# Kernel tuning notes

Measured on AMD Instinct MI355X. Metric: run time of the kernel, lower is better.

## Reference

```python
import jax, jax.numpy as jnp
import numpy as np

N_ENT = 500000
N_REL = 64
E_DIM = 128
R_DIM = 128
REG_LAMBDA = 1e-5
M = 8192


def setup_inputs() -> dict:
    key = jax.random.key(0)
    k1, k2, k3, k4, k5, k6, k7 = jax.random.split(key, 7)
    # Xavier-uniform-ish init for relation_weight; normal for embeddings (nn.Embedding default)
    gain = float(np.sqrt(2.0))  # calculate_gain('relu')
    bound = gain * float(np.sqrt(6.0 / (E_DIM + R_DIM)))
    return {
        "h": jax.random.randint(k1, (M,), 0, N_ENT),
        "r": jax.random.randint(k2, (M,), 0, N_REL),
        "pos_t": jax.random.randint(k3, (M,), 0, N_ENT),
        "neg_t": jax.random.randint(k4, (M,), 0, N_ENT),
        "entity_embed": jax.random.normal(k5, (N_ENT, E_DIM), dtype=jnp.float32),
        "relation_embed": jax.random.normal(k6, (N_REL, R_DIM), dtype=jnp.float32),
        "relation_weight": jax.random.uniform(k7, (N_REL, E_DIM, R_DIM), dtype=jnp.float32, minval=-bound, maxval=bound),
    }


def _l2_norm(x):
    # sum over feature dim, halved -> shape (M,)
    return jnp.sum(x * x, axis=1) / 2.0


def reference(h, r, pos_t, neg_t, entity_embed, relation_embed, relation_weight):
    h_embed = entity_embed[h]            # (M, E)
    r_embed = relation_embed[r]          # (M, R)
    pos_t_embed = entity_embed[pos_t]    # (M, E)
    neg_t_embed = entity_embed[neg_t]    # (M, E)

    W = relation_weight[r]               # (M, E, R) relation-indexed gather
    h_vec = jnp.einsum('me,mer->mr', h_embed, W)
    pos_t_vec = jnp.einsum('me,mer->mr', pos_t_embed, W)
    neg_t_vec = jnp.einsum('me,mer->mr', neg_t_embed, W)

    pos_score = _l2_norm(h_vec + r_embed - pos_t_vec)
    neg_score = _l2_norm(h_vec + r_embed - neg_t_vec)
    kg_loss = jnp.mean(-jax.nn.log_sigmoid(pos_score - neg_score))

    kg_reg_loss = (jnp.mean(_l2_norm(h_embed)) + jnp.mean(_l2_norm(r_embed))
                   + jnp.mean(_l2_norm(pos_t_embed)) + jnp.mean(_l2_norm(neg_t_embed)))
    return kg_loss + REG_LAMBDA * kg_reg_loss
```

## Files before the change

### kernel.cpp

```cpp
#include <hip/hip_runtime.h>
#include <math.h>

#define E_DIM 128
#define R_DIM 128
#define N_REL 64
#define REG_LAMBDA 1e-5f

#define NSEG 32
#define GMAX 8
#define LISTMAX 512

__global__ void __launch_bounds__(128)
kge_grouped_kernel(const int* __restrict__ h_idx, const int* __restrict__ r_idx,
                   const int* __restrict__ pt_idx, const int* __restrict__ nt_idx,
                   const float* __restrict__ ent,
                   const float* __restrict__ rel,
                   const float* __restrict__ W,
                   float* __restrict__ per_sample,
                   int M)
{
    const int t      = threadIdx.x;
    const int rel_id = blockIdx.x >> 5;
    const int seg    = blockIdx.x & (NSEG - 1);

    __shared__ int s_cnt;
    __shared__ int s_list[LISTMAX];
    __shared__ __align__(16) float sh[GMAX][E_DIM];
    __shared__ __align__(16) float sp[GMAX][E_DIM];
    __shared__ __align__(16) float sn[GMAX][E_DIM];
    __shared__ float wpart[3][GMAX][2];

    const int range = (M + NSEG - 1) / NSEG;
    const int m0 = seg * range;
    const int m1 = min(m0 + range, M);

    if (t == 0) s_cnt = 0;
    __syncthreads();
    for (int m = m0 + t; m < m1; m += 128) {
        if (r_idx[m] == rel_id) {
            int p = atomicAdd(&s_cnt, 1);
            s_list[p] = m;
        }
    }
    __syncthreads();
    const int cnt = s_cnt;
    if (cnt == 0) return;

    const float* __restrict__ Wr = W + (size_t)rel_id * (E_DIM * R_DIM);
    const float re = rel[(size_t)rel_id * R_DIM + t];

    for (int c0 = 0; c0 < cnt; c0 += GMAX) {
#pragma unroll
        for (int g = 0; g < GMAX; ++g) {
            int sl = c0 + g; if (sl > cnt - 1) sl = cnt - 1;
            int m = s_list[sl];
            sh[g][t] = ent[(size_t)h_idx[m]  * E_DIM + t];
            sp[g][t] = ent[(size_t)pt_idx[m] * E_DIM + t];
            sn[g][t] = ent[(size_t)nt_idx[m] * E_DIM + t];
        }
        __syncthreads();

        float ah[GMAX], ap[GMAX], an[GMAX];
#pragma unroll
        for (int g = 0; g < GMAX; ++g) { ah[g] = 0.f; ap[g] = 0.f; an[g] = 0.f; }

#pragma unroll 2
        for (int e0 = 0; e0 < E_DIM; e0 += 4) {
            float w0 = Wr[(size_t)(e0 + 0) * R_DIM + t];
            float w1 = Wr[(size_t)(e0 + 1) * R_DIM + t];
            float w2 = Wr[(size_t)(e0 + 2) * R_DIM + t];
            float w3 = Wr[(size_t)(e0 + 3) * R_DIM + t];
#pragma unroll
            for (int g = 0; g < GMAX; ++g) {
                float4 h4 = *(const float4*)&sh[g][e0];
                float4 p4 = *(const float4*)&sp[g][e0];
                float4 n4 = *(const float4*)&sn[g][e0];
                ah[g] = fmaf(h4.x, w0, ah[g]); ah[g] = fmaf(h4.y, w1, ah[g]);
                ah[g] = fmaf(h4.z, w2, ah[g]); ah[g] = fmaf(h4.w, w3, ah[g]);
                ap[g] = fmaf(p4.x, w0, ap[g]); ap[g] = fmaf(p4.y, w1, ap[g]);
                ap[g] = fmaf(p4.z, w2, ap[g]); ap[g] = fmaf(p4.w, w3, ap[g]);
                an[g] = fmaf(n4.x, w0, an[g]); an[g] = fmaf(n4.y, w1, an[g]);
                an[g] = fmaf(n4.z, w2, an[g]); an[g] = fmaf(n4.w, w3, an[g]);
            }
        }

#pragma unroll
        for (int g = 0; g < GMAX; ++g) {
            float he = sh[g][t], pe = sp[g][t], ne = sn[g][t];
            float a  = ah[g] + re;
            float dp = a - ap[g];
            float dn = a - an[g];
            float pos = dp * dp;
            float neg = dn * dn;
            float reg = he * he + re * re + pe * pe + ne * ne;
#pragma unroll
            for (int off = 32; off > 0; off >>= 1) {
                pos += __shfl_down(pos, off);
                neg += __shfl_down(neg, off);
                reg += __shfl_down(reg, off);
            }
            if ((t & 63) == 0) {
                int wv = t >> 6;
                wpart[0][g][wv] = pos; wpart[1][g][wv] = neg; wpart[2][g][wv] = reg;
            }
        }
        __syncthreads();
        if (t < GMAX && (c0 + t) < cnt) {
            float P = wpart[0][t][0] + wpart[0][t][1];
            float N = wpart[1][t][0] + wpart[1][t][1];
            float R = wpart[2][t][0] + wpart[2][t][1];
            float diff = 0.5f * (P - N);
            float z = -diff;
            float sp_v = fmaxf(z, 0.f) + log1pf(expf(-fabsf(z)));
            per_sample[s_list[c0 + t]] = sp_v + REG_LAMBDA * 0.5f * R;
        }
    }
}

__global__ void __launch_bounds__(256)
kge_reduce_kernel(const float* __restrict__ per_sample, float* __restrict__ out, int M)
{
    int t = threadIdx.x;
    float s = 0.f;
    for (int i = t; i < M; i += 256) s += per_sample[i];
#pragma unroll
    for (int off = 32; off > 0; off >>= 1) s += __shfl_down(s, off);
    __shared__ float part[4];
    if ((t & 63) == 0) part[t >> 6] = s;
    __syncthreads();
    if (t == 0) out[0] = (part[0] + part[1] + part[2] + part[3]) / (float)M;
}

extern "C" void kernel_launch(void* const* d_in, const int* in_sizes, int n_in,
                              void* d_out, int out_size, void* d_ws, size_t ws_size,
                              hipStream_t stream)
{
    const int*   h_idx  = (const int*)d_in[0];
    const int*   r_idx  = (const int*)d_in[1];
    const int*   pt_idx = (const int*)d_in[2];
    const int*   nt_idx = (const int*)d_in[3];
    const float* ent    = (const float*)d_in[4];
    const float* rel    = (const float*)d_in[5];
    const float* W      = (const float*)d_in[6];
    float* out = (float*)d_out;

    int M = in_sizes[0];
    float* per_sample = (float*)d_ws;

    kge_grouped_kernel<<<N_REL * NSEG, 128, 0, stream>>>(h_idx, r_idx, pt_idx, nt_idx,
                                                         ent, rel, W, per_sample, M);
    kge_reduce_kernel<<<1, 256, 0, stream>>>(per_sample, out, M);
}
```

Before: 371.0 us.

## Split E-dim across thread quarters with 4-wide output tiles and shared-memory reduction

```diff
diff --git a/kernel.cpp b/kernel.cpp
--- a/kernel.cpp
+++ b/kernel.cpp
@@ -6,29 +6,34 @@
 #define N_REL 64
 #define REG_LAMBDA 1e-5f
 
-#define NSEG 32
-#define GMAX 8
+#define NSEG 16
+#define GG 8
+#define GEPI 4
 #define LISTMAX 512
 
-__global__ void __launch_bounds__(128)
-kge_grouped_kernel(const int* __restrict__ h_idx, const int* __restrict__ r_idx,
-                   const int* __restrict__ pt_idx, const int* __restrict__ nt_idx,
-                   const float* __restrict__ ent,
-                   const float* __restrict__ rel,
-                   const float* __restrict__ W,
-                   float* __restrict__ per_sample,
-                   int M)
+__global__ void __launch_bounds__(128, 2)
+kge_grouped3(const int* __restrict__ h_idx, const int* __restrict__ r_idx,
+             const int* __restrict__ pt_idx, const int* __restrict__ nt_idx,
+             const float* __restrict__ ent,
+             const float* __restrict__ rel,
+             const float* __restrict__ W,
+             float* __restrict__ per_sample,
+             int M)
 {
     const int t      = threadIdx.x;
-    const int rel_id = blockIdx.x >> 5;
+    const int rel_id = blockIdx.x >> 4;
     const int seg    = blockIdx.x & (NSEG - 1);
+    const int q      = t >> 5;
+    const int u      = t & 31;
+    const int c4     = u << 2;
 
     __shared__ int s_cnt;
     __shared__ int s_list[LISTMAX];
-    __shared__ __align__(16) float sh[GMAX][E_DIM];
-    __shared__ __align__(16) float sp[GMAX][E_DIM];
-    __shared__ __align__(16) float sn[GMAX][E_DIM];
-    __shared__ float wpart[3][GMAX][2];
+    __shared__ __align__(16) float sh[GG][E_DIM];
+    __shared__ __align__(16) float sp[GG][E_DIM];
+    __shared__ __align__(16) float sn[GG][E_DIM];
+    __shared__ __align__(16) float epi[GEPI][3][4][E_DIM];
+    __shared__ float wpart[3][GG][2];
 
     const int range = (M + NSEG - 1) / NSEG;
     const int m0 = seg * range;
@@ -39,19 +44,19 @@
     for (int m = m0 + t; m < m1; m += 128) {
         if (r_idx[m] == rel_id) {
             int p = atomicAdd(&s_cnt, 1);
-            s_list[p] = m;
+            if (p < LISTMAX) s_list[p] = m;
         }
     }
     __syncthreads();
     const int cnt = s_cnt;
     if (cnt == 0) return;
 
-    const float* __restrict__ Wr = W + (size_t)rel_id * (E_DIM * R_DIM);
+    const float* __restrict__ Wq = W + (size_t)rel_id * (E_DIM * R_DIM);
     const float re = rel[(size_t)rel_id * R_DIM + t];
 
-    for (int c0 = 0; c0 < cnt; c0 += GMAX) {
+    for (int c0 = 0; c0 < cnt; c0 += GG) {
 #pragma unroll
-        for (int g = 0; g < GMAX; ++g) {
+        for (int g = 0; g < GG; ++g) {
             int sl = c0 + g; if (sl > cnt - 1) sl = cnt - 1;
             int m = s_list[sl];
             sh[g][t] = ent[(size_t)h_idx[m]  * E_DIM + t];
@@ -60,52 +65,86 @@
         }
         __syncthreads();
 
-        float ah[GMAX], ap[GMAX], an[GMAX];
+        float aH[GG][4], aP[GG][4], aN[GG][4];
 #pragma unroll
-        for (int g = 0; g < GMAX; ++g) { ah[g] = 0.f; ap[g] = 0.f; an[g] = 0.f; }
+        for (int g = 0; g < GG; ++g)
+#pragma unroll
+            for (int c = 0; c < 4; ++c) { aH[g][c] = 0.f; aP[g][c] = 0.f; aN[g][c] = 0.f; }
 
-#pragma unroll 2
-        for (int e0 = 0; e0 < E_DIM; e0 += 4) {
-            float w0 = Wr[(size_t)(e0 + 0) * R_DIM + t];
-            float w1 = Wr[(size_t)(e0 + 1) * R_DIM + t];
-            float w2 = Wr[(size_t)(e0 + 2) * R_DIM + t];
-            float w3 = Wr[(size_t)(e0 + 3) * R_DIM + t];
+        const int eBase = q << 5;
 #pragma unroll
-            for (int g = 0; g < GMAX; ++g) {
-                float4 h4 = *(const float4*)&sh[g][e0];
-                float4 p4 = *(const float4*)&sp[g][e0];
-                float4 n4 = *(const float4*)&sn[g][e0];
-                ah[g] = fmaf(h4.x, w0, ah[g]); ah[g] = fmaf(h4.y, w1, ah[g]);
-                ah[g] = fmaf(h4.z, w2, ah[g]); ah[g] = fmaf(h4.w, w3, ah[g]);
-                ap[g] = fmaf(p4.x, w0, ap[g]); ap[g] = fmaf(p4.y, w1, ap[g]);
-                ap[g] = fmaf(p4.z, w2, ap[g]); ap[g] = fmaf(p4.w, w3, ap[g]);
-                an[g] = fmaf(n4.x, w0, an[g]); an[g] = fmaf(n4.y, w1, an[g]);
-                an[g] = fmaf(n4.z, w2, an[g]); an[g] = fmaf(n4.w, w3, an[g]);
+        for (int es = 0; es < 8; ++es) {
+            const int e0 = eBase + (es << 2);
+            const float4 W0 = *(const float4*)&Wq[(size_t)(e0 + 0) * R_DIM + c4];
+            const float4 W1 = *(const float4*)&Wq[(size_t)(e0 + 1) * R_DIM + c4];
+            const float4 W2 = *(const float4*)&Wq[(size_t)(e0 + 2) * R_DIM + c4];
+            const float4 W3 = *(const float4*)&Wq[(size_t)(e0 + 3) * R_DIM + c4];
+            const float w0[4] = {W0.x, W0.y, W0.z, W0.w};
+            const float w1[4] = {W1.x, W1.y, W1.z, W1.w};
+            const float w2[4] = {W2.x, W2.y, W2.z, W2.w};
+            const float w3[4] = {W3.x, W3.y, W3.z, W3.w};
+#pragma unroll
+            for (int g = 0; g < GG; ++g) {
+                const float4 h4 = *(const float4*)&sh[g][e0];
+                const float4 p4 = *(const float4*)&sp[g][e0];
+                const float4 n4 = *(const float4*)&sn[g][e0];
+#pragma unroll
+                for (int c = 0; c < 4; ++c) {
+                    aH[g][c] = fmaf(h4.x, w0[c], aH[g][c]);
+                    aH[g][c] = fmaf(h4.y, w1[c], aH[g][c]);
+                    aH[g][c] = fmaf(h4.z, w2[c], aH[g][c]);
+                    aH[g][c] = fmaf(h4.w, w3[c], aH[g][c]);
+                    aP[g][c] = fmaf(p4.x, w0[c], aP[g][c]);
+                    aP[g][c] = fmaf(p4.y, w1[c], aP[g][c]);
+                    aP[g][c] = fmaf(p4.z, w2[c], aP[g][c]);
+                    aP[g][c] = fmaf(p4.w, w3[c], aP[g][c]);
+                    aN[g][c] = fmaf(n4.x, w0[c], aN[g][c]);
+                    aN[g][c] = fmaf(n4.y, w1[c], aN[g][c]);
+                    aN[g][c] = fmaf(n4.z, w2[c], aN[g][c]);
+                    aN[g][c] = fmaf(n4.w, w3[c], aN[g][c]);
+                }
             }
         }
 
 #pragma unroll
-        for (int g = 0; g < GMAX; ++g) {
-            float he = sh[g][t], pe = sp[g][t], ne = sn[g][t];
-            float a  = ah[g] + re;
-            float dp = a - ap[g];
-            float dn = a - an[g];
-            float pos = dp * dp;
-            float neg = dn * dn;
-            float reg = he * he + re * re + pe * pe + ne * ne;
+        for (int r0 = 0; r0 < GG; r0 += GEPI) {
+            __syncthreads();
 #pragma unroll
-            for (int off = 32; off > 0; off >>= 1) {
-                pos += __shfl_down(pos, off);
-                neg += __shfl_down(neg, off);
-                reg += __shfl_down(reg, off);
+            for (int g = 0; g < GEPI; ++g) {
+                const int gg = r0 + g;
+                *(float4*)&epi[g][0][q][c4] = make_float4(aH[gg][0], aH[gg][1], aH[gg][2], aH[gg][3]);
+                *(float4*)&epi[g][1][q][c4] = make_float4(aP[gg][0], aP[gg][1], aP[gg][2], aP[gg][3]);
+                *(float4*)&epi[g][2][q][c4] = make_float4(aN[gg][0], aN[gg][1], aN[gg][2], aN[gg][3]);
             }
-            if ((t & 63) == 0) {
-                int wv = t >> 6;
-                wpart[0][g][wv] = pos; wpart[1][g][wv] = neg; wpart[2][g][wv] = reg;
+            __syncthreads();
+#pragma unroll
+            for (int g = 0; g < GEPI; ++g) {
+                const int gg = r0 + g;
+                float hv = ((epi[g][0][0][t] + epi[g][0][1][t]) + epi[g][0][2][t]) + epi[g][0][3][t];
+                float pv = ((epi[g][1][0][t] + epi[g][1][1][t]) + epi[g][1][2][t]) + epi[g][1][3][t];
+                float nv = ((epi[g][2][0][t] + epi[g][2][1][t]) + epi[g][2][2][t]) + epi[g][2][3][t];
+                float he = sh[gg][t], pe = sp[gg][t], ne = sn[gg][t];
+                float a  = hv + re;
+                float dp = a - pv;
+                float dn = a - nv;
+                float pos = dp * dp;
+                float neg = dn * dn;
+                float reg = he * he + re * re + pe * pe + ne * ne;
+#pragma unroll
+                for (int off = 32; off > 0; off >>= 1) {
+                    pos += __shfl_down(pos, off);
+                    neg += __shfl_down(neg, off);
+                    reg += __shfl_down(reg, off);
+                }
+                if ((t & 63) == 0) {
+                    wpart[0][gg][t >> 6] = pos;
+                    wpart[1][gg][t >> 6] = neg;
+                    wpart[2][gg][t >> 6] = reg;
+                }
             }
         }
         __syncthreads();
-        if (t < GMAX && (c0 + t) < cnt) {
+        if (t < GG && (c0 + t) < cnt) {
             float P = wpart[0][t][0] + wpart[0][t][1];
             float N = wpart[1][t][0] + wpart[1][t][1];
             float R = wpart[2][t][0] + wpart[2][t][1];
@@ -147,7 +186,7 @@
     int M = in_sizes[0];
     float* per_sample = (float*)d_ws;
 
-    kge_grouped_kernel<<<N_REL * NSEG, 128, 0, stream>>>(h_idx, r_idx, pt_idx, nt_idx,
-                                                         ent, rel, W, per_sample, M);
+    kge_grouped3<<<N_REL * NSEG, 128, 0, stream>>>(h_idx, r_idx, pt_idx, nt_idx,
+                                                   ent, rel, W, per_sample, M);
     kge_reduce_kernel<<<1, 256, 0, stream>>>(per_sample, out, M);
 }
```

Result: slower. 527.1 us (+42.1%).

## Split E-dimension across four waves with shared-memory partial-sum reduction

Applied to the files above, without the earlier changes.

```diff
diff --git a/kernel.cpp b/kernel.cpp
--- a/kernel.cpp
+++ b/kernel.cpp
@@ -6,29 +6,33 @@
 #define N_REL 64
 #define REG_LAMBDA 1e-5f
 
-#define NSEG 32
-#define GMAX 8
-#define LISTMAX 512
+#define NSEG 16
+#define G 4
+#define LISTMAX 256
 
-__global__ void __launch_bounds__(128)
-kge_grouped_kernel(const int* __restrict__ h_idx, const int* __restrict__ r_idx,
-                   const int* __restrict__ pt_idx, const int* __restrict__ nt_idx,
-                   const float* __restrict__ ent,
-                   const float* __restrict__ rel,
-                   const float* __restrict__ W,
-                   float* __restrict__ per_sample,
-                   int M)
+__global__ void __launch_bounds__(256)
+kge_grouped4(const int* __restrict__ h_idx, const int* __restrict__ r_idx,
+             const int* __restrict__ pt_idx, const int* __restrict__ nt_idx,
+             const float* __restrict__ ent,
+             const float* __restrict__ rel,
+             const float* __restrict__ W,
+             float* __restrict__ per_sample,
+             int M)
 {
     const int t      = threadIdx.x;
-    const int rel_id = blockIdx.x >> 5;
+    const int rel_id = blockIdx.x >> 4;
     const int seg    = blockIdx.x & (NSEG - 1);
+    const int q      = t >> 6;
+    const int u      = t & 63;
+    const int cb     = u << 1;
 
     __shared__ int s_cnt;
     __shared__ int s_list[LISTMAX];
-    __shared__ __align__(16) float sh[GMAX][E_DIM];
-    __shared__ __align__(16) float sp[GMAX][E_DIM];
-    __shared__ __align__(16) float sn[GMAX][E_DIM];
-    __shared__ float wpart[3][GMAX][2];
+    __shared__ __align__(16) float sh[G][E_DIM];
+    __shared__ __align__(16) float sp[G][E_DIM];
+    __shared__ __align__(16) float sn[G][E_DIM];
+    __shared__ __align__(16) float epi[G][3][4][R_DIM];
+    __shared__ float wpart[3][G][2];
 
     const int range = (M + NSEG - 1) / NSEG;
     const int m0 = seg * range;
@@ -36,80 +40,122 @@
 
     if (t == 0) s_cnt = 0;
     __syncthreads();
-    for (int m = m0 + t; m < m1; m += 128) {
+    for (int m = m0 + t; m < m1; m += 256) {
         if (r_idx[m] == rel_id) {
             int p = atomicAdd(&s_cnt, 1);
-            s_list[p] = m;
+            if (p < LISTMAX) s_list[p] = m;
         }
     }
     __syncthreads();
-    const int cnt = s_cnt;
+    const int cnt = min(s_cnt, LISTMAX);
     if (cnt == 0) return;
 
-    const float* __restrict__ Wr = W + (size_t)rel_id * (E_DIM * R_DIM);
-    const float re = rel[(size_t)rel_id * R_DIM + t];
+    const float* __restrict__ Wq =
+        W + (size_t)rel_id * (E_DIM * R_DIM) + (size_t)(q << 5) * R_DIM + cb;
+    const float re = (t < E_DIM) ? rel[(size_t)rel_id * R_DIM + t] : 0.f;
 
-    for (int c0 = 0; c0 < cnt; c0 += GMAX) {
-#pragma unroll
-        for (int g = 0; g < GMAX; ++g) {
+    const int elem = t & 127;
+    const int half = t >> 7;
+
+    for (int c0 = 0; c0 < cnt; c0 += G) {
+        for (int g = half; g < G; g += 2) {
             int sl = c0 + g; if (sl > cnt - 1) sl = cnt - 1;
             int m = s_list[sl];
-            sh[g][t] = ent[(size_t)h_idx[m]  * E_DIM + t];
-            sp[g][t] = ent[(size_t)pt_idx[m] * E_DIM + t];
-            sn[g][t] = ent[(size_t)nt_idx[m] * E_DIM + t];
+            sh[g][elem] = ent[(size_t)h_idx[m]  * E_DIM + elem];
+            sp[g][elem] = ent[(size_t)pt_idx[m] * E_DIM + elem];
+            sn[g][elem] = ent[(size_t)nt_idx[m] * E_DIM + elem];
         }
         __syncthreads();
 
-        float ah[GMAX], ap[GMAX], an[GMAX];
+        float aH[G][2], aP[G][2], aN[G][2];
 #pragma unroll
-        for (int g = 0; g < GMAX; ++g) { ah[g] = 0.f; ap[g] = 0.f; an[g] = 0.f; }
+        for (int g = 0; g < G; ++g) {
+            aH[g][0] = 0.f; aH[g][1] = 0.f;
+            aP[g][0] = 0.f; aP[g][1] = 0.f;
+            aN[g][0] = 0.f; aN[g][1] = 0.f;
+        }
 
+        const int eBase = q << 5;
 #pragma unroll 2
-        for (int e0 = 0; e0 < E_DIM; e0 += 4) {
-            float w0 = Wr[(size_t)(e0 + 0) * R_DIM + t];
-            float w1 = Wr[(size_t)(e0 + 1) * R_DIM + t];
-            float w2 = Wr[(size_t)(e0 + 2) * R_DIM + t];
-            float w3 = Wr[(size_t)(e0 + 3) * R_DIM + t];
+        for (int es = 0; es < 8; ++es) {
+            const int e0 = eBase + (es << 2);
+            const float2 w0 = *(const float2*)(Wq + (size_t)((es << 2) + 0) * R_DIM);
+            const float2 w1 = *(const float2*)(Wq + (size_t)((es << 2) + 1) * R_DIM);
+            const float2 w2 = *(const float2*)(Wq + (size_t)((es << 2) + 2) * R_DIM);
+            const float2 w3 = *(const float2*)(Wq + (size_t)((es << 2) + 3) * R_DIM);
 #pragma unroll
-            for (int g = 0; g < GMAX; ++g) {
-                float4 h4 = *(const float4*)&sh[g][e0];
-                float4 p4 = *(const float4*)&sp[g][e0];
-                float4 n4 = *(const float4*)&sn[g][e0];
-                ah[g] = fmaf(h4.x, w0, ah[g]); ah[g] = fmaf(h4.y, w1, ah[g]);
-                ah[g] = fmaf(h4.z, w2, ah[g]); ah[g] = fmaf(h4.w, w3, ah[g]);
-                ap[g] = fmaf(p4.x, w0, ap[g]); ap[g] = fmaf(p4.y, w1, ap[g]);
-                ap[g] = fmaf(p4.z, w2, ap[g]); ap[g] = fmaf(p4.w, w3, ap[g]);
-                an[g] = fmaf(n4.x, w0, an[g]); an[g] = fmaf(n4.y, w1, an[g]);
-                an[g] = fmaf(n4.z, w2, an[g]); an[g] = fmaf(n4.w, w3, an[g]);
+            for (int g = 0; g < G; ++g) {
+                const float4 h4 = *(const float4*)&sh[g][e0];
+                const float4 p4 = *(const float4*)&sp[g][e0];
+                const float4 n4 = *(const float4*)&sn[g][e0];
+                aH[g][0] = fmaf(h4.x, w0.x, aH[g][0]);
+                aH[g][0] = fmaf(h4.y, w1.x, aH[g][0]);
+                aH[g][0] = fmaf(h4.z, w2.x, aH[g][0]);
+                aH[g][0] = fmaf(h4.w, w3.x, aH[g][0]);
+                aH[g][1] = fmaf(h4.x, w0.y, aH[g][1]);
+                aH[g][1] = fmaf(h4.y, w1.y, aH[g][1]);
+                aH[g][1] = fmaf(h4.z, w2.y, aH[g][1]);
+                aH[g][1] = fmaf(h4.w, w3.y, aH[g][1]);
+                aP[g][0] = fmaf(p4.x, w0.x, aP[g][0]);
+                aP[g][0] = fmaf(p4.y, w1.x, aP[g][0]);
+                aP[g][0] = fmaf(p4.z, w2.x, aP[g][0]);
+                aP[g][0] = fmaf(p4.w, w3.x, aP[g][0]);
+                aP[g][1] = fmaf(p4.x, w0.y, aP[g][1]);
+                aP[g][1] = fmaf(p4.y, w1.y, aP[g][1]);
+                aP[g][1] = fmaf(p4.z, w2.y, aP[g][1]);
+                aP[g][1] = fmaf(p4.w, w3.y, aP[g][1]);
+                aN[g][0] = fmaf(n4.x, w0.x, aN[g][0]);
+                aN[g][0] = fmaf(n4.y, w1.x, aN[g][0]);
+                aN[g][0] = fmaf(n4.z, w2.x, aN[g][0]);
+                aN[g][0] = fmaf(n4.w, w3.x, aN[g][0]);
+                aN[g][1] = fmaf(n4.x, w0.y, aN[g][1]);
+                aN[g][1] = fmaf(n4.y, w1.y, aN[g][1]);
+                aN[g][1] = fmaf(n4.z, w2.y, aN[g][1]);
+                aN[g][1] = fmaf(n4.w, w3.y, aN[g][1]);
             }
         }
 
 #pragma unroll
-        for (int g = 0; g < GMAX; ++g) {
-            float he = sh[g][t], pe = sp[g][t], ne = sn[g][t];
-            float a  = ah[g] + re;
-            float dp = a - ap[g];
-            float dn = a - an[g];
-            float pos = dp * dp;
-            float neg = dn * dn;
-            float reg = he * he + re * re + pe * pe + ne * ne;
+        for (int g = 0; g < G; ++g) {
+            *(float2*)&epi[g][0][q][cb] = make_float2(aH[g][0], aH[g][1]);
+            *(float2*)&epi[g][1][q][cb] = make_float2(aP[g][0], aP[g][1]);
+            *(float2*)&epi[g][2][q][cb] = make_float2(aN[g][0], aN[g][1]);
+        }
+        __syncthreads();
+
+        if (t < E_DIM) {
 #pragma unroll
-            for (int off = 32; off > 0; off >>= 1) {
-                pos += __shfl_down(pos, off);
-                neg += __shfl_down(neg, off);
-                reg += __shfl_down(reg, off);
-            }
-            if ((t & 63) == 0) {
-                int wv = t >> 6;
-                wpart[0][g][wv] = pos; wpart[1][g][wv] = neg; wpart[2][g][wv] = reg;
+            for (int g = 0; g < G; ++g) {
+                float hv = (epi[g][0][0][t] + epi[g][0][1][t]) + (epi[g][0][2][t] + epi[g][0][3][t]);
+                float pv = (epi[g][1][0][t] + epi[g][1][1][t]) + (epi[g][1][2][t] + epi[g][1][3][t]);
+                float nv = (epi[g][2][0][t] + epi[g][2][1][t]) + (epi[g][2][2][t] + epi[g][2][3][t]);
+                float he = sh[g][t], pe = sp[g][t], ne = sn[g][t];
+                float a  = hv + re;
+                float dp = a - pv;
+                float dn = a - nv;
+                float pos = dp * dp;
+                float neg = dn * dn;
+                float reg = he * he + re * re + pe * pe + ne * ne;
+#pragma unroll
+                for (int off = 32; off > 0; off >>= 1) {
+                    pos += __shfl_down(pos, off);
+                    neg += __shfl_down(neg, off);
+                    reg += __shfl_down(reg, off);
+                }
+                if ((t & 63) == 0) {
+                    wpart[0][g][t >> 6] = pos;
+                    wpart[1][g][t >> 6] = neg;
+                    wpart[2][g][t >> 6] = reg;
+                }
             }
         }
         __syncthreads();
-        if (t < GMAX && (c0 + t) < cnt) {
-            float P = wpart[0][t][0] + wpart[0][t][1];
-            float N = wpart[1][t][0] + wpart[1][t][1];
-            float R = wpart[2][t][0] + wpart[2][t][1];
-            float diff = 0.5f * (P - N);
+
+        if (t < G && (c0 + t) < cnt) {
+            float P  = wpart[0][t][0] + wpart[0][t][1];
+            float Nn = wpart[1][t][0] + wpart[1][t][1];
+            float R  = wpart[2][t][0] + wpart[2][t][1];
+            float diff = 0.5f * (P - Nn);
             float z = -diff;
             float sp_v = fmaxf(z, 0.f) + log1pf(expf(-fabsf(z)));
             per_sample[s_list[c0 + t]] = sp_v + REG_LAMBDA * 0.5f * R;
@@ -147,7 +193,7 @@
     int M = in_sizes[0];
     float* per_sample = (float*)d_ws;
 
-    kge_grouped_kernel<<<N_REL * NSEG, 128, 0, stream>>>(h_idx, r_idx, pt_idx, nt_idx,
-                                                         ent, rel, W, per_sample, M);
+    kge_grouped4<<<N_REL * NSEG, 256, 0, stream>>>(h_idx, r_idx, pt_idx, nt_idx,
+                                                   ent, rel, W, per_sample, M);
     kge_reduce_kernel<<<1, 256, 0, stream>>>(per_sample, out, M);
 }
```

Measured after the change: 340.8 us. -8.1%, faster.
